# Performance work log

Hardware: AMD Instinct MI355X
Metric: run time of the kernel (lower is better)

Reference implementation:

```python
import jax, jax.numpy as jnp
import numpy as np

HIDDEN = 2048
NUM_HEADS = 32
HEAD_DIM = 64
NUM_KV = 8
GROUP = NUM_HEADS // NUM_KV
SCALE = HEAD_DIM ** -0.5
ROPE_BASE = 10000.0


def apply_rope(t):
    # t: [B, H, S, D]; standard half-split rotary embedding
    S, D = t.shape[-2], t.shape[-1]
    inv_freq = 1.0 / (ROPE_BASE ** (jnp.arange(0, D, 2, dtype=jnp.float32) / D))  # [D/2]
    ang = jnp.arange(S, dtype=jnp.float32)[:, None] * inv_freq[None, :]           # [S, D/2]
    cos, sin = jnp.cos(ang), jnp.sin(ang)
    x1, x2 = t[..., : D // 2], t[..., D // 2 :]
    return jnp.concatenate([x1 * cos - x2 * sin, x2 * cos + x1 * sin], axis=-1)


def setup_inputs() -> dict:
    key = jax.random.key(0)
    ks = jax.random.split(key, 10)
    B, S = 2, 2048
    s_in = HIDDEN ** -0.5
    s_o = (NUM_HEADS * HEAD_DIM) ** -0.5
    return {
        "x": jax.random.normal(ks[0], (B, S, HIDDEN), jnp.float32),
        "Wq": jax.random.normal(ks[1], (NUM_HEADS * HEAD_DIM, HIDDEN), jnp.float32) * s_in,
        "bq": jnp.zeros((NUM_HEADS * HEAD_DIM,), jnp.float32),
        "Wk": jax.random.normal(ks[2], (NUM_KV * HEAD_DIM, HIDDEN), jnp.float32) * s_in,
        "bk": jnp.zeros((NUM_KV * HEAD_DIM,), jnp.float32),
        "Wv": jax.random.normal(ks[3], (NUM_KV * HEAD_DIM, HIDDEN), jnp.float32) * s_in,
        "bv": jnp.zeros((NUM_KV * HEAD_DIM,), jnp.float32),
        "Wo": jax.random.normal(ks[4], (HIDDEN, NUM_HEADS * HEAD_DIM), jnp.float32) * s_o,
        "bo": jnp.zeros((HIDDEN,), jnp.float32),
        "key_weights": jax.random.normal(ks[5], (NUM_HEADS,), jnp.float32),
    }


def reference(x, Wq, bq, Wk, bk, Wv, bv, Wo, bo, key_weights):
    B, S, _ = x.shape
    q = (x @ Wq.T + bq).reshape(B, S, NUM_HEADS, HEAD_DIM).transpose(0, 2, 1, 3)
    k = (x @ Wk.T + bk).reshape(B, S, NUM_KV, HEAD_DIM).transpose(0, 2, 1, 3)
    v = (x @ Wv.T + bv).reshape(B, S, NUM_KV, HEAD_DIM).transpose(0, 2, 1, 3)
    q = apply_rope(q)
    k = apply_rope(k)
    # group queries per KV head: [B, kv, g, S, D]
    qg = q.reshape(B, NUM_KV, GROUP, S, HEAD_DIM)
    scores = jnp.einsum("bkgsd,bktd->bkgst", qg, k) * SCALE
    scores = scores * key_weights.reshape(1, NUM_KV, GROUP, 1, 1)
    causal = jnp.tril(jnp.ones((S, S), bool))
    scores = jnp.where(causal, scores, -jnp.inf)
    a = jax.nn.softmax(scores, axis=-1)
    o = jnp.einsum("bkgst,bktd->bkgsd", a, v)  # [B, kv, g, S, D]
    o = o.reshape(B, NUM_HEADS, S, HEAD_DIM).transpose(0, 2, 1, 3).reshape(B, S, NUM_HEADS * HEAD_DIM)
    return o @ Wo.T + bo
```

## Files before the change

kernel.cpp:

```cpp
#include <hip/hip_runtime.h>
#include <stdint.h>

#define S_LEN 2048
#define HID   2048
#define NH    32
#define NKV   8
#define HD    64
#define BATCH 2
#define NROWS (BATCH * S_LEN)
#define QKVN  (NH*HD + 2*NKV*HD)

typedef unsigned short u16;
typedef __bf16 bf16_t;
typedef bf16_t bf16x8 __attribute__((ext_vector_type(8)));
typedef float  f32x4  __attribute__((ext_vector_type(4)));
typedef float  f32x16 __attribute__((ext_vector_type(16)));
typedef u16    u16x8  __attribute__((ext_vector_type(8)));

#define LOG2E 1.4426950408889634f

__device__ __forceinline__ u16 f2bf(float f) {
    union { float f; uint32_t u; } v; v.f = f;
    uint32_t u = v.u;
    return (u16)((u + 0x7fffu + ((u >> 16) & 1u)) >> 16);
}

__device__ __forceinline__ unsigned cvtpk(float a, float b) {
    unsigned r;
    asm("v_cvt_pk_bf16_f32 %0, %1, %2" : "=v"(r) : "v"(a), "v"(b));
    return r;
}

__device__ __forceinline__ void plswap(unsigned &a, unsigned &b) {
    asm volatile("v_permlane32_swap_b32 %0, %1" : "+v"(a), "+v"(b));
}

__device__ __forceinline__ void llds16(const void* g, void* l) {
    __builtin_amdgcn_global_load_lds(
        (const __attribute__((address_space(1))) void*)g,
        (__attribute__((address_space(3))) void*)l,
        16, 0, 0);
}

__device__ __forceinline__ unsigned swz(unsigned row) {
    return ((row ^ (row >> 2)) & 3u) << 4;
}

#define SB()    __builtin_amdgcn_sched_barrier(0)
#define BAR()   __builtin_amdgcn_s_barrier()

#define CBAR(N) do { \
    asm volatile("s_waitcnt vmcnt(" #N ")" ::: "memory"); \
    __builtin_amdgcn_s_barrier(); \
    __builtin_amdgcn_sched_barrier(0); \
} while (0)

#define CVT_GROUPS 2359296
__global__ void prep_all(const float* __restrict__ x, const float* __restrict__ wq,
                         const float* __restrict__ wk, const float* __restrict__ wv,
                         const float* __restrict__ wo,
                         const float* __restrict__ bq, const float* __restrict__ bk,
                         const float* __restrict__ bv,
                         u16* __restrict__ xb, u16* __restrict__ wqkvb, u16* __restrict__ wob,
                         float* __restrict__ rtab, float* __restrict__ bqkv) {
    int e = blockIdx.x * 256 + threadIdx.x;
    if (e < CVT_GROUPS) {
        const float* s; u16* d; int o;
        if (e < 1048576)      { s = x;  d = xb;                 o = e; }
        else if (e < 1572864) { s = wq; d = wqkvb;              o = e - 1048576; }
        else if (e < 1703936) { s = wk; d = wqkvb + 2048*2048;  o = e - 1572864; }
        else if (e < 1835008) { s = wv; d = wqkvb + 2560*2048;  o = e - 1703936; }
        else                  { s = wo; d = wob;                o = e - 1835008; }
        const float4* sp = (const float4*)s;
        float4 a = sp[2*(size_t)o], b = sp[2*(size_t)o + 1];
        u16x8 r;
        r[0]=f2bf(a.x); r[1]=f2bf(a.y); r[2]=f2bf(a.z); r[3]=f2bf(a.w);
        r[4]=f2bf(b.x); r[5]=f2bf(b.y); r[6]=f2bf(b.z); r[7]=f2bf(b.w);
        *(u16x8*)(d + 8*(size_t)o) = r;
    } else if (e < CVT_GROUPS + 65536) {
        int idx = e - CVT_GROUPS;
        int i = idx & 31, s = idx >> 5;
        float invf = exp2f(-(float)i * (13.287712379549449f / 32.0f));
        float ang = (float)s * invf;
        float sn, cs;
        sincosf(ang, &sn, &cs);
        rtab[idx] = cs;
        rtab[S_LEN*32 + idx] = sn;
    } else if (e < CVT_GROUPS + 65536 + QKVN) {
        int i = e - CVT_GROUPS - 65536;
        bqkv[i] = (i < 2048) ? bq[i] : (i < 2560 ? bk[i - 2048] : bv[i - 2560]);
    }
}


__global__ __launch_bounds__(256, 3) void gemm_qkv(
    const u16* __restrict__ A, const u16* __restrict__ Bw,
    const float* __restrict__ bias, const float* __restrict__ rtab,
    const float* __restrict__ kw,
    u16* __restrict__ qpk, u16* __restrict__ kpk, u16* __restrict__ vlin)
{
    const int K = HID;
    const int nbn = QKVN >> 7;
    const int nwg = (NROWS >> 7) * nbn;
    int wg = blockIdx.x;
    wg = (wg & 7) * (nwg >> 3) + (wg >> 3);
    const int bm = wg / nbn, bn = wg % nbn;
    const int brow = bm << 7, bcol = bn << 7;

    __shared__ u16 sbuf[3][8192];

    const int t = threadIdx.x;
    const int lane = t & 63, wid = t >> 6;
    const int wr = wid >> 1, wn = wid & 1;
    const int lq = lane & 31, hi = lane >> 5;

    auto stageAll = [&](int kt, int bi) {
        const int k0 = kt << 5;
        #pragma unroll
        for (int i = 0; i < 2; ++i) {
            const unsigned off = ((unsigned)t << 4) + ((unsigned)i << 12);
            const unsigned row = off >> 6;
            const unsigned scb = (off & 63) ^ swz(row);
            llds16(A + (size_t)(brow + row) * K + (k0 + (scb >> 1)), &sbuf[bi][0] + (off >> 1));
        }
        #pragma unroll
        for (int i = 0; i < 2; ++i) {
            const unsigned off = ((unsigned)t << 4) + ((unsigned)i << 12);
            const unsigned row = off >> 6;
            const unsigned scb = (off & 63) ^ swz(row);
            llds16(Bw + (size_t)(bcol + row) * K + (k0 + (scb >> 1)), &sbuf[bi][4096] + (off >> 1));
        }
    };

    f32x16 acc[2][2] = {};
    const int nk = K >> 5;

    stageAll(0, 0);
    stageAll(1, 1);
    int cur = 0, st2 = 2;
    for (int kt = 0; kt < nk; ++kt) {
        if (kt + 1 < nk) asm volatile("s_waitcnt vmcnt(4)" ::: "memory");
        else             asm volatile("s_waitcnt vmcnt(0)" ::: "memory");
        BAR();
        SB();
        const char* sA = (const char*)&sbuf[cur][0];
        const char* sB = (const char*)&sbuf[cur][4096];
        bf16x8 af[4], bfv[4];
        #pragma unroll
        for (int mt = 0; mt < 2; ++mt)
            #pragma unroll
            for (int s = 0; s < 2; ++s) {
                const unsigned row = wr*64 + mt*32 + lq;
                af[mt*2+s] = *(const bf16x8*)(sA + row*64 + ((unsigned)(32*s + 16*hi) ^ swz(row)));
            }
        #pragma unroll
        for (int s = 0; s < 2; ++s) {
            const unsigned row = wn*64 + lq;
            bfv[s] = *(const bf16x8*)(sB + row*64 + ((unsigned)(32*s + 16*hi) ^ swz(row)));
        }
        SB();
        #pragma unroll
        for (int s = 0; s < 2; ++s) {
            const unsigned row = wn*64 + 32 + lq;
            bfv[2+s] = *(const bf16x8*)(sB + row*64 + ((unsigned)(32*s + 16*hi) ^ swz(row)));
        }
        SB();
        if (kt + 2 < nk) stageAll(kt + 2, st2);
        asm volatile("s_waitcnt lgkmcnt(2)" ::: "memory");
        SB();
        __builtin_amdgcn_s_setprio(1);
        #pragma unroll
        for (int mt = 0; mt < 2; ++mt)
            #pragma unroll
            for (int s = 0; s < 2; ++s)
                acc[mt][0] = __builtin_amdgcn_mfma_f32_32x32x16_bf16(af[mt*2+s], bfv[s], acc[mt][0], 0, 0, 0);
        __builtin_amdgcn_s_setprio(0);
        asm volatile("s_waitcnt lgkmcnt(0)" ::: "memory");
        SB();
        __builtin_amdgcn_s_setprio(1);
        #pragma unroll
        for (int mt = 0; mt < 2; ++mt)
            #pragma unroll
            for (int s = 0; s < 2; ++s)
                acc[mt][1] = __builtin_amdgcn_mfma_f32_32x32x16_bf16(af[mt*2+s], bfv[2+s], acc[mt][1], 0, 0, 0);
        __builtin_amdgcn_s_setprio(0);
        cur = (cur == 2) ? 0 : cur + 1;
        st2 = (st2 == 2) ? 0 : st2 + 1;
    }

    const int rowb = brow + wr*64;
    const int c64 = bcol + wn*64;
    const int hb  = c64 >> 6;
    if (hb < 40) {
        const bool isQ = hb < 32;
        const float sc = isQ ? (0.125f * LOG2E * kw[hb]) : 1.0f;
        u16* dst = isQ ? qpk : kpk;
        const int nheads = isQ ? 32 : 8;
        const int hloc = isQ ? hb : (hb - 32);
        const float b1 = bias[c64 + lq];
        const float b2 = bias[c64 + 32 + lq];
        #pragma unroll
        for (int mt = 0; mt < 2; ++mt) {
            #pragma unroll
            for (int r = 0; r < 16; ++r) {
                const int row = rowb + mt*32 + (r & 3) + 8*(r >> 2) + 4*hi;
                const int s = row & (S_LEN - 1);
                const int bb = row >> 11;
                const float x1 = acc[mt][0][r] + b1;
                const float x2 = acc[mt][1][r] + b2;
                const float c = rtab[s*32 + lq];
                const float sn = rtab[S_LEN*32 + s*32 + lq];
                const size_t base = ((size_t)(bb*nheads + hloc)) * (S_LEN*64) + (size_t)s*64;
                dst[base + lq]      = f2bf((x1*c - x2*sn) * sc);
                dst[base + lq + 32] = f2bf((x2*c + x1*sn) * sc);
            }
        }
    } else {
        #pragma unroll
        for (int nt = 0; nt < 2; ++nt) {
            const int col = c64 + nt*32 + lq;
            const float bv = bias[col];
            #pragma unroll
            for (int mt = 0; mt < 2; ++mt)
                #pragma unroll
                for (int r = 0; r < 16; ++r) {
                    const int row = rowb + mt*32 + (r & 3) + 8*(r >> 2) + 4*hi;
                    vlin[(size_t)row * 512 + (col - 2560)] = f2bf(acc[mt][nt][r] + bv);
                }
        }
    }
}

__global__ __launch_bounds__(256, 3) void gemm_bt(
    const u16* __restrict__ A, const u16* __restrict__ Bw,
    const float* __restrict__ bias, float* __restrict__ C,
    int M, int N, int K)
{
    const int nbn = N >> 7;
    const int nwg = (M >> 7) * nbn;
    int wg = blockIdx.x;
    wg = (wg & 7) * (nwg >> 3) + (wg >> 3);
    const int bm = wg / nbn, bn = wg % nbn;
    const int brow = bm << 7, bcol = bn << 7;

    __shared__ u16 sbuf[3][8192];

    const int t = threadIdx.x;
    const int lane = t & 63, wid = t >> 6;
    const int wr = wid >> 1, wn = wid & 1;
    const int lq = lane & 31, hi = lane >> 5;

    auto stageAll = [&](int kt, int bi) {
        const int k0 = kt << 5;
        #pragma unroll
        for (int i = 0; i < 2; ++i) {
            const unsigned off = ((unsigned)t << 4) + ((unsigned)i << 12);
            const unsigned row = off >> 6;
            const unsigned scb = (off & 63) ^ swz(row);
            llds16(A + (size_t)(brow + row) * K + (k0 + (scb >> 1)), &sbuf[bi][0] + (off >> 1));
        }
        #pragma unroll
        for (int i = 0; i < 2; ++i) {
            const unsigned off = ((unsigned)t << 4) + ((unsigned)i << 12);
            const unsigned row = off >> 6;
            const unsigned scb = (off & 63) ^ swz(row);
            llds16(Bw + (size_t)(bcol + row) * K + (k0 + (scb >> 1)), &sbuf[bi][4096] + (off >> 1));
        }
    };

    f32x16 acc[2][2] = {};
    const int nk = K >> 5;

    stageAll(0, 0);
    stageAll(1, 1);
    int cur = 0, st2 = 2;
    for (int kt = 0; kt < nk; ++kt) {
        if (kt + 1 < nk) asm volatile("s_waitcnt vmcnt(4)" ::: "memory");
        else             asm volatile("s_waitcnt vmcnt(0)" ::: "memory");
        BAR();
        SB();
        const char* sA = (const char*)&sbuf[cur][0];
        const char* sB = (const char*)&sbuf[cur][4096];
        bf16x8 af[4], bfv[4];
        #pragma unroll
        for (int mt = 0; mt < 2; ++mt)
            #pragma unroll
            for (int s = 0; s < 2; ++s) {
                const unsigned row = wr*64 + mt*32 + lq;
                af[mt*2+s] = *(const bf16x8*)(sA + row*64 + ((unsigned)(32*s + 16*hi) ^ swz(row)));
            }
        #pragma unroll
        for (int s = 0; s < 2; ++s) {
            const unsigned row = wn*64 + lq;
            bfv[s] = *(const bf16x8*)(sB + row*64 + ((unsigned)(32*s + 16*hi) ^ swz(row)));
        }
        SB();
        #pragma unroll
        for (int s = 0; s < 2; ++s) {
            const unsigned row = wn*64 + 32 + lq;
            bfv[2+s] = *(const bf16x8*)(sB + row*64 + ((unsigned)(32*s + 16*hi) ^ swz(row)));
        }
        SB();
        if (kt + 2 < nk) stageAll(kt + 2, st2);
        asm volatile("s_waitcnt lgkmcnt(2)" ::: "memory");
        SB();
        __builtin_amdgcn_s_setprio(1);
        #pragma unroll
        for (int mt = 0; mt < 2; ++mt)
            #pragma unroll
            for (int s = 0; s < 2; ++s)
                acc[mt][0] = __builtin_amdgcn_mfma_f32_32x32x16_bf16(af[mt*2+s], bfv[s], acc[mt][0], 0, 0, 0);
        __builtin_amdgcn_s_setprio(0);
        asm volatile("s_waitcnt lgkmcnt(0)" ::: "memory");
        SB();
        __builtin_amdgcn_s_setprio(1);
        #pragma unroll
        for (int mt = 0; mt < 2; ++mt)
            #pragma unroll
            for (int s = 0; s < 2; ++s)
                acc[mt][1] = __builtin_amdgcn_mfma_f32_32x32x16_bf16(af[mt*2+s], bfv[2+s], acc[mt][1], 0, 0, 0);
        __builtin_amdgcn_s_setprio(0);
        cur = (cur == 2) ? 0 : cur + 1;
        st2 = (st2 == 2) ? 0 : st2 + 1;
    }

    #pragma unroll
    for (int mt = 0; mt < 2; ++mt)
        #pragma unroll
        for (int nt = 0; nt < 2; ++nt) {
            const int col = bcol + wn*64 + nt*32 + lq;
            const float bv = bias[col];
            #pragma unroll
            for (int r = 0; r < 16; ++r) {
                const int row = brow + wr*64 + mt*32 + (r & 3) + 8*(r >> 2) + 4*hi;
                C[(size_t)row * N + col] = acc[mt][nt][r] + bv;
            }
        }
}

__global__ void pack_vt(const u16* __restrict__ vlin, u16* __restrict__ vtb) {
    __shared__ u16 tile[64][67];
    const int st = blockIdx.x;
    const int bk = blockIdx.y;
    const int t = threadIdx.x;
    const int b = bk >> 3, kvh = bk & 7;
    const int r = t >> 2, cg = (t & 3) << 4;
    const u16* src = vlin + ((size_t)(b*S_LEN + st*64 + r)) * 512 + kvh*64 + cg;
    #pragma unroll
    for (int j = 0; j < 16; ++j) tile[r][cg + j] = src[j];
    __syncthreads();
    const int d = t >> 2, sg = (t & 3) << 4;
    u16* dst = vtb + ((size_t)(bk*64 + d)) * S_LEN + st*64 + sg;
    #pragma unroll
    for (int j = 0; j < 16; ++j) dst[j] = tile[sg + j][d];
}

__global__ __launch_bounds__(512, 4) void attn_fwd(
    const u16* __restrict__ Q,
    const u16* __restrict__ Kk,
    const u16* __restrict__ Vt,
    u16* __restrict__ O)
{
    __shared__ u16 sK[3][64 * 64];
    __shared__ u16 sV[3][64 * 64];

    const int t = threadIdx.x;
    const int lane = t & 63, wid = t >> 6;
    const int hi = lane >> 5, lq = lane & 31;
    const int bid = blockIdx.x;
    const int qb = (bid < 256) ? (7 - (bid >> 6)) : ((bid >> 6) - 4);
    const int bh = bid & 63;
    const int b = bh >> 5, h = bh & 31;
    const int kvh = h >> 2;

    const u16* Kp = Kk + ((size_t)(b*NKV + kvh)) * (S_LEN * 64);
    const u16* Vp = Vt + ((size_t)(b*NKV + kvh)) * (64 * S_LEN);

    const int q0w = qb*256 + wid*32;
    const int qg  = q0w + lq;

    const u16* Qrow = Q + (((size_t)bh) * S_LEN + qg) * 64 + 8*hi;
    bf16x8 qf[4];
    #pragma unroll
    for (int kd = 0; kd < 4; ++kd)
        qf[kd] = *(const bf16x8*)(Qrow + 16*kd);

    f32x16 accO0 = {}, accO1 = {};
    float m_run = 0.f, l_run = 0.f;

    const int ntB = 4*qb + 4;
    const int tmax_w = (q0w + 31) >> 6;

    auto stageKV = [&](int kt, int bi) {
        const int kv = kt << 6;
        const unsigned row = t >> 3, cb = (t & 7) << 4;
        const unsigned scb = cb ^ ((row & 7) << 4);
        llds16(Kp + (size_t)(kv + row) * 64 + (scb >> 1), &sK[bi][0] + t*8);
        llds16(Vp + (size_t)row * S_LEN + kv + (scb >> 1), &sV[bi][0] + t*8);
    };

    stageKV(0, 0);
    stageKV(1, 1);
    int cur = 0, st2 = 2;

    for (int tt = 0; tt < ntB; ++tt) {
        if (tt < ntB - 1) CBAR(2); else CBAR(0);
        if (tt + 2 < ntB) stageKV(tt + 2, st2);
        if (tt <= tmax_w) {
            const int kv0 = tt * 64;
            const float nm = -m_run;
            f32x16 s0, s1;
            #pragma unroll
            for (int r = 0; r < 16; ++r) { s0[r] = nm; s1[r] = nm; }
            __builtin_amdgcn_s_setprio(1);
            #pragma unroll
            for (int kd = 0; kd < 4; ++kd) {
                const unsigned bc = ((unsigned)(32*kd + 16*hi)) ^ ((lq & 7) << 4);
                bf16x8 k0 = *(const bf16x8*)((const char*)&sK[cur][0] + lq*128 + bc);
                bf16x8 k1 = *(const bf16x8*)((const char*)&sK[cur][0] + (32 + lq)*128 + bc);
                s0 = __builtin_amdgcn_mfma_f32_32x32x16_bf16(k0, qf[kd], s0, 0, 0, 0);
                s1 = __builtin_amdgcn_mfma_f32_32x32x16_bf16(k1, qf[kd], s1, 0, 0, 0);
            }
            __builtin_amdgcn_s_setprio(0);
            if (kv0 + 63 > q0w) {
                #pragma unroll
                for (int r = 0; r < 16; ++r) {
                    const int kvg = kv0 + (r & 3) + 8*(r >> 2) + 4*hi;
                    if (kvg > qg)      s0[r] = -INFINITY;
                    if (kvg + 32 > qg) s1[r] = -INFINITY;
                }
            }
            float mx[8];
            #pragma unroll
            for (int r = 0; r < 8; ++r)
                mx[r] = fmaxf(fmaxf(s0[r], s0[r+8]), fmaxf(s1[r], s1[r+8]));
            float tm = fmaxf(fmaxf(fmaxf(mx[0], mx[1]), fmaxf(mx[2], mx[3])),
                             fmaxf(fmaxf(mx[4], mx[5]), fmaxf(mx[6], mx[7])));
            tm = fmaxf(tm, __shfl_xor(tm, 32));
            if (!__all(tm <= 8.0f)) {
                const float dd = fmaxf(tm, 0.f);
                const float al = __builtin_amdgcn_exp2f(-dd);
                m_run += dd;
                l_run *= al;
                #pragma unroll
                for (int r = 0; r < 16; ++r) { accO0[r] *= al; accO1[r] *= al; }
                #pragma unroll
                for (int r = 0; r < 16; ++r) { s0[r] -= dd; s1[r] -= dd; }
            }
            #pragma unroll
            for (int r = 0; r < 16; ++r) {
                s0[r] = __builtin_amdgcn_exp2f(s0[r]);
                s1[r] = __builtin_amdgcn_exp2f(s1[r]);
            }
            float sm[8];
            #pragma unroll
            for (int r = 0; r < 8; ++r)
                sm[r] = (s0[r] + s0[r+8]) + (s1[r] + s1[r+8]);
            float rs = ((sm[0]+sm[1]) + (sm[2]+sm[3])) + ((sm[4]+sm[5]) + (sm[6]+sm[7]));
            rs += __shfl_xor(rs, 32);
            l_run += rs;

            #pragma unroll
            for (int ks = 0; ks < 4; ++ks) {
                const f32x16& e = (ks & 2) ? s1 : s0;
                const int rb = (ks & 1) * 8;
                unsigned x0 = cvtpk(e[rb + 0], e[rb + 1]);
                unsigned x1 = cvtpk(e[rb + 2], e[rb + 3]);
                unsigned y0 = cvtpk(e[rb + 4], e[rb + 5]);
                unsigned y1 = cvtpk(e[rb + 6], e[rb + 7]);
                plswap(x0, y0);
                plswap(x1, y1);
                union { unsigned u[4]; bf16x8 v; } pb;
                pb.u[0] = x0; pb.u[1] = x1; pb.u[2] = y0; pb.u[3] = y1;
                const unsigned bc = ((unsigned)(32*ks + 16*hi)) ^ ((lq & 7) << 4);
                bf16x8 v0 = *(const bf16x8*)((const char*)&sV[cur][0] + lq*128 + bc);
                bf16x8 v1 = *(const bf16x8*)((const char*)&sV[cur][0] + (32 + lq)*128 + bc);
                __builtin_amdgcn_s_setprio(1);
                accO0 = __builtin_amdgcn_mfma_f32_32x32x16_bf16(v0, pb.v, accO0, 0, 0, 0);
                accO1 = __builtin_amdgcn_mfma_f32_32x32x16_bf16(v1, pb.v, accO1, 0, 0, 0);
                __builtin_amdgcn_s_setprio(0);
            }
        }
        cur = (cur == 2) ? 0 : cur + 1;
        st2 = (st2 == 2) ? 0 : st2 + 1;
    }

    const float inv = 1.0f / l_run;
    u16* orow = O + (((size_t)(b * S_LEN) + q0w + lq)) * (NH*HD) + h*64;
    #pragma unroll
    for (int g = 0; g < 4; ++g) {
        uint2 w0, w1;
        w0.x = cvtpk(accO0[4*g + 0] * inv, accO0[4*g + 1] * inv);
        w0.y = cvtpk(accO0[4*g + 2] * inv, accO0[4*g + 3] * inv);
        *(uint2*)(orow + 8*g + 4*hi) = w0;
        w1.x = cvtpk(accO1[4*g + 0] * inv, accO1[4*g + 1] * inv);
        w1.y = cvtpk(accO1[4*g + 2] * inv, accO1[4*g + 3] * inv);
        *(uint2*)(orow + 32 + 8*g + 4*hi) = w1;
    }
}

extern "C" void kernel_launch(void* const* d_in, const int* in_sizes, int n_in,
                              void* d_out, int out_size, void* d_ws, size_t ws_size,
                              hipStream_t stream) {
    const float* x  = (const float*)d_in[0];
    const float* Wq = (const float*)d_in[1];
    const float* bq = (const float*)d_in[2];
    const float* Wk = (const float*)d_in[3];
    const float* bk = (const float*)d_in[4];
    const float* Wv = (const float*)d_in[5];
    const float* bv = (const float*)d_in[6];
    const float* Wo = (const float*)d_in[7];
    const float* bo = (const float*)d_in[8];
    const float* kw = (const float*)d_in[9];

    uint8_t* ws = (uint8_t*)d_ws;
    u16*   xb    = (u16*)(ws);
    u16*   wqkvb = (u16*)(ws + 16777216);
    u16*   wob   = (u16*)(ws + 29360128);
    u16*   qpk   = (u16*)(ws + 37748736);
    u16*   kpk   = (u16*)(ws + 54525952);
    u16*   vlin  = (u16*)(ws + 58720256);
    u16*   vtb   = (u16*)(ws + 62914560);
    u16*   ob    = (u16*)(ws + 67108864);
    float* bqkv  = (float*)(ws + 83886080);
    float* rtab  = (float*)(ws + 83898368);

    prep_all<<<9484, 256, 0, stream>>>(x, Wq, Wk, Wv, Wo, bq, bk, bv,
                                       xb, wqkvb, wob, rtab, bqkv);

    gemm_qkv<<<768, 256, 0, stream>>>(xb, wqkvb, bqkv, rtab, kw, qpk, kpk, vlin);

    pack_vt<<<dim3(32, 16), 256, 0, stream>>>(vlin, vtb);

    attn_fwd<<<dim3(512), dim3(512), 0, stream>>>(qpk, kpk, vtb, ob);

    gemm_bt<<<512, 256, 0, stream>>>(ob, wob, bo, (float*)d_out, NROWS, HID, HID);

    (void)in_sizes; (void)n_in; (void)out_size; (void)ws_size;
}
```

Measured before the change: 188.1 us.

## Give each GEMM wave private LDS tiles and drop block barriers

Both GEMM kernels now let each wave load its own 64-row A and B slices into a private LDS region, double-buffered, so the per-iteration workgroup barrier is removed and waves run independently. The cost is redundant global loads: A rows are loaded by two waves and B rows by two waves, doubling global/L2 traffic per block, and LDS use grows so launch bounds drop occupancy from 3 to 2 blocks. The prefetch is moved after the first MFMA batch, once the current buffer's reads have completed.

```diff
diff --git a/kernel.cpp b/kernel.cpp
--- a/kernel.cpp
+++ b/kernel.cpp
@@ -93,7 +93,7 @@
 }
 
 
-__global__ __launch_bounds__(256, 3) void gemm_qkv(
+__global__ __launch_bounds__(256, 2) void gemm_qkv(
     const u16* __restrict__ A, const u16* __restrict__ Bw,
     const float* __restrict__ bias, const float* __restrict__ rtab,
     const float* __restrict__ kw,
@@ -107,65 +107,65 @@
     const int bm = wg / nbn, bn = wg % nbn;
     const int brow = bm << 7, bcol = bn << 7;
 
-    __shared__ u16 sbuf[3][8192];
+    __shared__ u16 sbuf[2][4][4096];
 
     const int t = threadIdx.x;
     const int lane = t & 63, wid = t >> 6;
-    const int wr = wid >> 1, wn = wid & 1;
+    const int wm = wid >> 1, wn = wid & 1;
     const int lq = lane & 31, hi = lane >> 5;
 
-    auto stageAll = [&](int kt, int bi) {
+    const int arow0 = brow + wm*64;
+    const int brow0 = bcol + wn*64;
+    const unsigned rl = ((unsigned)lane) >> 2;
+    const unsigned cb = ((unsigned)lane & 3) << 4;
+
+    auto stage = [&](int kt, int bi) {
         const int k0 = kt << 5;
-        #pragma unroll
-        for (int i = 0; i < 2; ++i) {
-            const unsigned off = ((unsigned)t << 4) + ((unsigned)i << 12);
-            const unsigned row = off >> 6;
-            const unsigned scb = (off & 63) ^ swz(row);
-            llds16(A + (size_t)(brow + row) * K + (k0 + (scb >> 1)), &sbuf[bi][0] + (off >> 1));
-        }
-        #pragma unroll
-        for (int i = 0; i < 2; ++i) {
-            const unsigned off = ((unsigned)t << 4) + ((unsigned)i << 12);
-            const unsigned row = off >> 6;
-            const unsigned scb = (off & 63) ^ swz(row);
-            llds16(Bw + (size_t)(bcol + row) * K + (k0 + (scb >> 1)), &sbuf[bi][4096] + (off >> 1));
+        u16* wb = &sbuf[bi][wid][0];
+        #pragma unroll
+        for (int i = 0; i < 4; ++i) {
+            const unsigned r = i*16 + rl;
+            const unsigned scb = cb ^ swz(r);
+            llds16(A + (size_t)(arow0 + r) * K + (k0 + (scb >> 1)), wb + ((i*1024 + lane*16) >> 1));
+        }
+        #pragma unroll
+        for (int i = 0; i < 4; ++i) {
+            const unsigned r = i*16 + rl;
+            const unsigned scb = cb ^ swz(r);
+            llds16(Bw + (size_t)(brow0 + r) * K + (k0 + (scb >> 1)), wb + 2048 + ((i*1024 + lane*16) >> 1));
         }
     };
 
     f32x16 acc[2][2] = {};
     const int nk = K >> 5;
 
-    stageAll(0, 0);
-    stageAll(1, 1);
-    int cur = 0, st2 = 2;
+    stage(0, 0);
+    stage(1, 1);
     for (int kt = 0; kt < nk; ++kt) {
-        if (kt + 1 < nk) asm volatile("s_waitcnt vmcnt(4)" ::: "memory");
+        if (kt + 1 < nk) asm volatile("s_waitcnt vmcnt(8)" ::: "memory");
         else             asm volatile("s_waitcnt vmcnt(0)" ::: "memory");
-        BAR();
-        SB();
-        const char* sA = (const char*)&sbuf[cur][0];
-        const char* sB = (const char*)&sbuf[cur][4096];
+        SB();
+        const char* sA = (const char*)&sbuf[kt & 1][wid][0];
+        const char* sB = sA + 4096;
         bf16x8 af[4], bfv[4];
         #pragma unroll
         for (int mt = 0; mt < 2; ++mt)
             #pragma unroll
             for (int s = 0; s < 2; ++s) {
-                const unsigned row = wr*64 + mt*32 + lq;
+                const unsigned row = mt*32 + lq;
                 af[mt*2+s] = *(const bf16x8*)(sA + row*64 + ((unsigned)(32*s + 16*hi) ^ swz(row)));
             }
         #pragma unroll
         for (int s = 0; s < 2; ++s) {
-            const unsigned row = wn*64 + lq;
+            const unsigned row = lq;
             bfv[s] = *(const bf16x8*)(sB + row*64 + ((unsigned)(32*s + 16*hi) ^ swz(row)));
         }
-        SB();
         #pragma unroll
         for (int s = 0; s < 2; ++s) {
-            const unsigned row = wn*64 + 32 + lq;
+            const unsigned row = 32 + lq;
             bfv[2+s] = *(const bf16x8*)(sB + row*64 + ((unsigned)(32*s + 16*hi) ^ swz(row)));
         }
         SB();
-        if (kt + 2 < nk) stageAll(kt + 2, st2);
         asm volatile("s_waitcnt lgkmcnt(2)" ::: "memory");
         SB();
         __builtin_amdgcn_s_setprio(1);
@@ -177,6 +177,7 @@
         __builtin_amdgcn_s_setprio(0);
         asm volatile("s_waitcnt lgkmcnt(0)" ::: "memory");
         SB();
+        if (kt + 2 < nk) stage(kt + 2, kt & 1);
         __builtin_amdgcn_s_setprio(1);
         #pragma unroll
         for (int mt = 0; mt < 2; ++mt)
@@ -184,11 +185,9 @@
             for (int s = 0; s < 2; ++s)
                 acc[mt][1] = __builtin_amdgcn_mfma_f32_32x32x16_bf16(af[mt*2+s], bfv[2+s], acc[mt][1], 0, 0, 0);
         __builtin_amdgcn_s_setprio(0);
-        cur = (cur == 2) ? 0 : cur + 1;
-        st2 = (st2 == 2) ? 0 : st2 + 1;
     }
 
-    const int rowb = brow + wr*64;
+    const int rowb = brow + wm*64;
     const int c64 = bcol + wn*64;
     const int hb  = c64 >> 6;
     if (hb < 40) {
@@ -231,7 +230,7 @@
     }
 }
 
-__global__ __launch_bounds__(256, 3) void gemm_bt(
+__global__ __launch_bounds__(256, 2) void gemm_bt(
     const u16* __restrict__ A, const u16* __restrict__ Bw,
     const float* __restrict__ bias, float* __restrict__ C,
     int M, int N, int K)
@@ -243,65 +242,65 @@
     const int bm = wg / nbn, bn = wg % nbn;
     const int brow = bm << 7, bcol = bn << 7;
 
-    __shared__ u16 sbuf[3][8192];
+    __shared__ u16 sbuf[2][4][4096];
 
     const int t = threadIdx.x;
     const int lane = t & 63, wid = t >> 6;
-    const int wr = wid >> 1, wn = wid & 1;
+    const int wm = wid >> 1, wn = wid & 1;
     const int lq = lane & 31, hi = lane >> 5;
 
-    auto stageAll = [&](int kt, int bi) {
+    const int arow0 = brow + wm*64;
+    const int brow0 = bcol + wn*64;
+    const unsigned rl = ((unsigned)lane) >> 2;
+    const unsigned cb = ((unsigned)lane & 3) << 4;
+
+    auto stage = [&](int kt, int bi) {
         const int k0 = kt << 5;
-        #pragma unroll
-        for (int i = 0; i < 2; ++i) {
-            const unsigned off = ((unsigned)t << 4) + ((unsigned)i << 12);
-            const unsigned row = off >> 6;
-            const unsigned scb = (off & 63) ^ swz(row);
-            llds16(A + (size_t)(brow + row) * K + (k0 + (scb >> 1)), &sbuf[bi][0] + (off >> 1));
-        }
-        #pragma unroll
-        for (int i = 0; i < 2; ++i) {
-            const unsigned off = ((unsigned)t << 4) + ((unsigned)i << 12);
-            const unsigned row = off >> 6;
-            const unsigned scb = (off & 63) ^ swz(row);
-            llds16(Bw + (size_t)(bcol + row) * K + (k0 + (scb >> 1)), &sbuf[bi][4096] + (off >> 1));
+        u16* wb = &sbuf[bi][wid][0];
+        #pragma unroll
+        for (int i = 0; i < 4; ++i) {
+            const unsigned r = i*16 + rl;
+            const unsigned scb = cb ^ swz(r);
+            llds16(A + (size_t)(arow0 + r) * K + (k0 + (scb >> 1)), wb + ((i*1024 + lane*16) >> 1));
+        }
+        #pragma unroll
+        for (int i = 0; i < 4; ++i) {
+            const unsigned r = i*16 + rl;
+            const unsigned scb = cb ^ swz(r);
+            llds16(Bw + (size_t)(brow0 + r) * K + (k0 + (scb >> 1)), wb + 2048 + ((i*1024 + lane*16) >> 1));
         }
     };
 
     f32x16 acc[2][2] = {};
     const int nk = K >> 5;
 
-    stageAll(0, 0);
-    stageAll(1, 1);
-    int cur = 0, st2 = 2;
+    stage(0, 0);
+    stage(1, 1);
     for (int kt = 0; kt < nk; ++kt) {
-        if (kt + 1 < nk) asm volatile("s_waitcnt vmcnt(4)" ::: "memory");
+        if (kt + 1 < nk) asm volatile("s_waitcnt vmcnt(8)" ::: "memory");
         else             asm volatile("s_waitcnt vmcnt(0)" ::: "memory");
-        BAR();
-        SB();
-        const char* sA = (const char*)&sbuf[cur][0];
-        const char* sB = (const char*)&sbuf[cur][4096];
+        SB();
+        const char* sA = (const char*)&sbuf[kt & 1][wid][0];
+        const char* sB = sA + 4096;
         bf16x8 af[4], bfv[4];
         #pragma unroll
         for (int mt = 0; mt < 2; ++mt)
             #pragma unroll
             for (int s = 0; s < 2; ++s) {
-                const unsigned row = wr*64 + mt*32 + lq;
+                const unsigned row = mt*32 + lq;
                 af[mt*2+s] = *(const bf16x8*)(sA + row*64 + ((unsigned)(32*s + 16*hi) ^ swz(row)));
             }
         #pragma unroll
         for (int s = 0; s < 2; ++s) {
-            const unsigned row = wn*64 + lq;
+            const unsigned row = lq;
             bfv[s] = *(const bf16x8*)(sB + row*64 + ((unsigned)(32*s + 16*hi) ^ swz(row)));
         }
-        SB();
         #pragma unroll
         for (int s = 0; s < 2; ++s) {
-            const unsigned row = wn*64 + 32 + lq;
+            const unsigned row = 32 + lq;
             bfv[2+s] = *(const bf16x8*)(sB + row*64 + ((unsigned)(32*s + 16*hi) ^ swz(row)));
         }
         SB();
-        if (kt + 2 < nk) stageAll(kt + 2, st2);
         asm volatile("s_waitcnt lgkmcnt(2)" ::: "memory");
         SB();
         __builtin_amdgcn_s_setprio(1);
@@ -313,6 +312,7 @@
         __builtin_amdgcn_s_setprio(0);
         asm volatile("s_waitcnt lgkmcnt(0)" ::: "memory");
         SB();
+        if (kt + 2 < nk) stage(kt + 2, kt & 1);
         __builtin_amdgcn_s_setprio(1);
         #pragma unroll
         for (int mt = 0; mt < 2; ++mt)
@@ -320,8 +320,6 @@
             for (int s = 0; s < 2; ++s)
                 acc[mt][1] = __builtin_amdgcn_mfma_f32_32x32x16_bf16(af[mt*2+s], bfv[2+s], acc[mt][1], 0, 0, 0);
         __builtin_amdgcn_s_setprio(0);
-        cur = (cur == 2) ? 0 : cur + 1;
-        st2 = (st2 == 2) ? 0 : st2 + 1;
     }
 
     #pragma unroll
@@ -332,7 +330,7 @@
             const float bv = bias[col];
             #pragma unroll
             for (int r = 0; r < 16; ++r) {
-                const int row = brow + wr*64 + mt*32 + (r & 3) + 8*(r >> 2) + 4*hi;
+                const int row = brow + wm*64 + mt*32 + (r & 3) + 8*(r >> 2) + 4*hi;
                 C[(size_t)row * N + col] = acc[mt][nt][r] + bv;
             }
         }
```

After: 230.6 us. 1.23x slower.
